# Performance work log

Hardware: AMD Instinct MI355X
Metric: run time of the kernel (lower is better)

The kernel has to match this reference:

```python
import jax, jax.numpy as jnp
import numpy as np

E_EDGES = 100000   # number of original edges (edge tokens)
M_PAIRS = 1000000  # number of edge-edge (line-graph) pairs
IN_DIM = 128
H = 8   # num_heads
D = 16  # out_dim per head


def setup_inputs() -> dict:
    key = jax.random.key(0)
    ks = jax.random.split(key, 8)
    edge_attr = jax.random.normal(ks[0], (E_EDGES, IN_DIM), dtype=jnp.float32)
    edge_edge_index = jax.random.randint(ks[1], (2, M_PAIRS), 0, E_EDGES, dtype=jnp.int64)
    s = 1.0 / np.sqrt(IN_DIM)  # xavier-ish scale
    Wq = jax.random.normal(ks[2], (IN_DIM, H * D), dtype=jnp.float32) * s
    Wk = jax.random.normal(ks[3], (IN_DIM, H * D), dtype=jnp.float32) * s
    Wv = jax.random.normal(ks[4], (IN_DIM, H * D), dtype=jnp.float32) * s
    bq = jnp.zeros((H * D,), dtype=jnp.float32)
    bk = jnp.zeros((H * D,), dtype=jnp.float32)
    bv = jnp.zeros((H * D,), dtype=jnp.float32)
    Aw = jax.random.normal(ks[5], (D, H), dtype=jnp.float32) * (1.0 / np.sqrt(D))
    return {"edge_attr": edge_attr, "edge_edge_index": edge_edge_index,
            "Wq": Wq, "bq": bq, "Wk": Wk, "bk": bk, "Wv": Wv, "bv": bv, "Aw": Aw}


def reference(edge_attr, edge_edge_index, Wq, bq, Wk, bk, Wv, bv, Aw):
    E = edge_attr.shape[0]
    # Q/K/V projections, reshaped to [E, H, D]
    Qh = (edge_attr @ Wq + bq).reshape(E, H, D)
    Kh = (edge_attr @ Wk + bk).reshape(E, H, D)
    Vh = (edge_attr @ Wv + bv).reshape(E, H, D)
    src = edge_edge_index[0]
    dst = edge_edge_index[1]
    # gather + additive score over edge-edge pairs: [M, H, D]
    score_vec = Kh[src] + Qh[dst]  # act = Identity
    # einsum 'ehd,dhc->ehc' with c=1 -> [M, H]
    raw_attn = jnp.einsum('mhd,dh->mh', score_vec, Aw)
    # segment softmax grouped by destination edge
    mx = jax.ops.segment_max(raw_attn, dst, num_segments=E)  # [E, H]
    ex = jnp.exp(raw_attn - mx[dst])
    denom = jax.ops.segment_sum(ex, dst, num_segments=E)[dst] + 1e-16
    attn = ex / denom  # [M, H]; dropout p=0 -> identity
    # weighted scatter-add aggregation
    msg = Vh[src] * attn[..., None]  # [M, H, D]
    edge_out = jax.ops.segment_sum(msg, dst, num_segments=E)  # [E, H, D]
    return edge_out
```

## Files before the change

kernel.cpp:

```cpp
#include <hip/hip_runtime.h>
#include <math.h>

static constexpr int E = 100000;
static constexpr int M = 1000000;

#define O_FLAG   0
#define O_WEFF   512
#define O_BKEFF  4608
#define O_BSWZ   5120
#define O_COUNTS 38400
#define O_OFFS   438784
#define O_BSUM   838784
#define O_BSUM2  840832
#define O_POS    842880
#define O_CSR    4842880
#define O_KS     8842880
#define O_VH     12042880
#define WS_NEEDED (O_VH + (size_t)E * 128 * 2)

typedef float f32x4 __attribute__((ext_vector_type(4)));
typedef short s16x8 __attribute__((ext_vector_type(8)));

__device__ __forceinline__ unsigned short f2bf(float f) {
    unsigned u = __float_as_uint(f);
    u += 0x7fffu + ((u >> 16) & 1u);
    return (unsigned short)(u >> 16);
}
__device__ __forceinline__ float bflo(unsigned u) { return __uint_as_float(u << 16); }
__device__ __forceinline__ float bfhi(unsigned u) { return __uint_as_float(u & 0xffff0000u); }

__global__ void k_prep(const float* __restrict__ Wk, const float* __restrict__ bk,
                       const float* __restrict__ Aw, const float* __restrict__ Wv,
                       const int* __restrict__ idx32, int* __restrict__ counts,
                       int* __restrict__ flag, float* __restrict__ weff,
                       float* __restrict__ bkeff, unsigned short* __restrict__ Bswz,
                       int nbE) {
    int bid = blockIdx.x, t = threadIdx.x;
    if (bid < nbE) {
        int i = bid * 256 + t;
        if (i < E) counts[i] = 0;
        return;
    }
    if (bid == nbE) {
        if (t < 128) {
            for (int h = 0; h < 8; h++) {
                float s = 0.f;
                for (int d = 0; d < 16; d++) s += Wk[t * 128 + h * 16 + d] * Aw[d * 8 + h];
                weff[t * 8 + h] = s;
            }
            if (t < 8) {
                float s = 0.f;
                for (int d = 0; d < 16; d++) s += bk[t * 16 + d] * Aw[d * 8 + t];
                bkeff[t] = s;
            }
        }
        return;
    }
    if (bid == nbE + 1) {
        if (t == 0) {
            int z = 0;
            for (int i = 0; i < 64; i++) z += (idx32[2 * i + 1] == 0) ? 1 : 0;
            *flag = (z == 64) ? 1 : 0;
        }
        return;
    }
    int p = (bid - (nbE + 2)) * 256 + t;
    int f = p >> 6, lane = p & 63;
    int c = f >> 3, tt = f & 7;
    int quad = lane >> 4, nn = lane & 15;
#pragma unroll
    for (int j = 0; j < 8; j++) {
        int k = c * 32 + quad * 8 + j;
        Bswz[p * 8 + j] = f2bf(Wv[k * 128 + tt * 16 + nn]);
    }
}

__global__ void k_count(const void* __restrict__ idx, const int* __restrict__ flagp,
                        int* __restrict__ counts, int* __restrict__ pos) {
    int m = blockIdx.x * blockDim.x + threadIdx.x;
    if (m >= M) return;
    int d = (*flagp) ? (int)((const long long*)idx)[M + m] : ((const int*)idx)[M + m];
    pos[m] = atomicAdd(&counts[d], 1);
}

__global__ void k_scanA(const int* __restrict__ counts, int* __restrict__ offs,
                        int* __restrict__ bsum) {
    __shared__ int sm[256];
    int tid = threadIdx.x;
    int i = blockIdx.x * 256 + tid;
    int v = (i < E) ? counts[i] : 0;
    sm[tid] = v;
    __syncthreads();
    for (int off = 1; off < 256; off <<= 1) {
        int add = (tid >= off) ? sm[tid - off] : 0;
        __syncthreads();
        sm[tid] += add;
        __syncthreads();
    }
    if (i < E) offs[i] = sm[tid] - v;
    if (tid == 255) bsum[blockIdx.x] = sm[255];
}

__global__ void k_scanB(const int* __restrict__ bsum, int* __restrict__ bsum2, int nb) {
    __shared__ int sm[512];
    int tid = threadIdx.x;
    int v = (tid < nb) ? bsum[tid] : 0;
    sm[tid] = v;
    __syncthreads();
    for (int off = 1; off < 512; off <<= 1) {
        int add = (tid >= off) ? sm[tid - off] : 0;
        __syncthreads();
        sm[tid] += add;
        __syncthreads();
    }
    bsum2[tid] = sm[tid] - v;
}

__global__ void k_fill(const void* __restrict__ idx, const int* __restrict__ flagp,
                       const int* __restrict__ offs, const int* __restrict__ bsum2,
                       const int* __restrict__ pos, int* __restrict__ csr) {
    int m = blockIdx.x * blockDim.x + threadIdx.x;
    if (m >= M) return;
    int s, d;
    if (*flagp) {
        const long long* p = (const long long*)idx;
        s = (int)p[m]; d = (int)p[M + m];
    } else {
        const int* p = (const int*)idx;
        s = p[m]; d = p[M + m];
    }
    csr[offs[d] + bsum2[d >> 8] + pos[m]] = s;
}

__global__ __launch_bounds__(256) void k_proj(
    const float* __restrict__ A, const short* __restrict__ Bswz,
    const float* __restrict__ bv, const float* __restrict__ weff,
    const float* __restrict__ bkeff, unsigned short* __restrict__ Vh,
    float* __restrict__ ksb) {
    __shared__ float we[1024];
    int t = threadIdx.x;
    ((float4*)we)[t] = ((const float4*)weff)[t & 255];
    __syncthreads();

    int lane = t & 63, wid = t >> 6;
    int rowbase = blockIdx.x * 64 + wid * 16;
    int quad = lane >> 4, nn = lane & 15;
    int m = rowbase + nn;
    int mc = (m < E) ? m : (E - 1);

    f32x4 acc[8];
#pragma unroll
    for (int tt = 0; tt < 8; tt++) acc[tt] = (f32x4){0.f, 0.f, 0.f, 0.f};
    float p[8];
#pragma unroll
    for (int h = 0; h < 8; h++) p[h] = 0.f;

#pragma unroll
    for (int c = 0; c < 4; c++) {
        const float4* ap = (const float4*)(A + (size_t)mc * 128 + c * 32 + quad * 8);
        float4 f0 = ap[0], f1 = ap[1];
        float a[8] = {f0.x, f0.y, f0.z, f0.w, f1.x, f1.y, f1.z, f1.w};
#pragma unroll
        for (int j = 0; j < 8; j++) {
            int k = c * 32 + quad * 8 + j;
            float4 w0 = *(const float4*)&we[k * 8];
            float4 w1 = *(const float4*)&we[k * 8 + 4];
            p[0] += a[j] * w0.x; p[1] += a[j] * w0.y;
            p[2] += a[j] * w0.z; p[3] += a[j] * w0.w;
            p[4] += a[j] * w1.x; p[5] += a[j] * w1.y;
            p[6] += a[j] * w1.z; p[7] += a[j] * w1.w;
        }
        s16x8 afrag;
#pragma unroll
        for (int j = 0; j < 8; j++) afrag[j] = (short)f2bf(a[j]);
#pragma unroll
        for (int tt = 0; tt < 8; tt++) {
            s16x8 bfrag = *(const s16x8*)(Bswz + (((c * 8 + tt) * 64 + lane) << 3));
            acc[tt] = __builtin_amdgcn_mfma_f32_16x16x32_bf16(afrag, bfrag, acc[tt], 0, 0, 0);
        }
    }
#pragma unroll
    for (int off = 16; off <= 32; off <<= 1)
#pragma unroll
        for (int h = 0; h < 8; h++) p[h] += __shfl_xor(p[h], off, 64);
    if (quad == 0 && m < E) {
        float4* op = (float4*)(ksb + (size_t)m * 8);
        op[0] = make_float4(p[0] + bkeff[0], p[1] + bkeff[1], p[2] + bkeff[2], p[3] + bkeff[3]);
        op[1] = make_float4(p[4] + bkeff[4], p[5] + bkeff[5], p[6] + bkeff[6], p[7] + bkeff[7]);
    }
#pragma unroll
    for (int tt = 0; tt < 8; tt++) {
        float bvc = bv[tt * 16 + nn];
#pragma unroll
        for (int r = 0; r < 4; r++) {
            int row = rowbase + quad * 4 + r;
            if (row < E)
                Vh[(size_t)row * 128 + tt * 16 + nn] = f2bf(acc[tt][r] + bvc);
        }
    }
}

__global__ __launch_bounds__(256) void k_seg(
    const float* __restrict__ ksb, const unsigned short* __restrict__ Vh,
    const int* __restrict__ offs, const int* __restrict__ bsum2,
    const int* __restrict__ csr, float* __restrict__ out) {
    int t = threadIdx.x;
    int h = t & 7;
    int seg = blockIdx.x * 32 + (t >> 3);
    int beg = offs[seg] + bsum2[seg >> 8];
    int end = (seg + 1 < E) ? (offs[seg + 1] + bsum2[(seg + 1) >> 8]) : M;
    int n = end - beg;
    const float* kb = ksb + h;

    float acc[16];
#pragma unroll
    for (int j = 0; j < 16; j++) acc[j] = 0.f;
    float l = 0.f;

    if (n > 0) {
        float mx = -INFINITY;
        for (int i = 0; i < n; i++) {
            int s = csr[beg + i];
            mx = fmaxf(mx, kb[(size_t)s * 8]);
        }
        for (int i = 0; i < n; i++) {
            int s = csr[beg + i];
            float w = __expf(kb[(size_t)s * 8] - mx);
            l += w;
            const uint4* vp = (const uint4*)(Vh + (size_t)s * 128 + h * 16);
            uint4 v0 = vp[0], v1 = vp[1];
            acc[0]  += bflo(v0.x) * w; acc[1]  += bfhi(v0.x) * w;
            acc[2]  += bflo(v0.y) * w; acc[3]  += bfhi(v0.y) * w;
            acc[4]  += bflo(v0.z) * w; acc[5]  += bfhi(v0.z) * w;
            acc[6]  += bflo(v0.w) * w; acc[7]  += bfhi(v0.w) * w;
            acc[8]  += bflo(v1.x) * w; acc[9]  += bfhi(v1.x) * w;
            acc[10] += bflo(v1.y) * w; acc[11] += bfhi(v1.y) * w;
            acc[12] += bflo(v1.z) * w; acc[13] += bfhi(v1.z) * w;
            acc[14] += bflo(v1.w) * w; acc[15] += bfhi(v1.w) * w;
        }
    }
    float inv = 1.0f / (l + 1e-16f);
    float4* op = (float4*)(out + (size_t)seg * 128 + h * 16);
#pragma unroll
    for (int j = 0; j < 4; j++)
        op[j] = make_float4(acc[4 * j] * inv, acc[4 * j + 1] * inv,
                            acc[4 * j + 2] * inv, acc[4 * j + 3] * inv);
}

extern "C" void kernel_launch(void* const* d_in, const int* in_sizes, int n_in,
                              void* d_out, int out_size, void* d_ws, size_t ws_size,
                              hipStream_t stream) {
    const float* edge_attr = (const float*)d_in[0];
    const void*  eei       = d_in[1];
    const float* Wk = (const float*)d_in[4];
    const float* bk = (const float*)d_in[5];
    const float* Wv = (const float*)d_in[6];
    const float* bv = (const float*)d_in[7];
    const float* Aw = (const float*)d_in[8];
    float* out = (float*)d_out;

    if (ws_size < WS_NEEDED) return;

    char* ws = (char*)d_ws;
    int*   flag   = (int*)(ws + O_FLAG);
    float* weff   = (float*)(ws + O_WEFF);
    float* bkeff  = (float*)(ws + O_BKEFF);
    unsigned short* Bswz = (unsigned short*)(ws + O_BSWZ);
    int*   counts = (int*)(ws + O_COUNTS);
    int*   offs   = (int*)(ws + O_OFFS);
    int*   bsum   = (int*)(ws + O_BSUM);
    int*   bsum2  = (int*)(ws + O_BSUM2);
    int*   pos    = (int*)(ws + O_POS);
    int*   csr    = (int*)(ws + O_CSR);
    float* ksb    = (float*)(ws + O_KS);
    unsigned short* Vh = (unsigned short*)(ws + O_VH);

    const int nbE = (E + 255) / 256;
    const int nbM = (M + 255) / 256;

    k_prep<<<nbE + 10, 256, 0, stream>>>(Wk, bk, Aw, Wv, (const int*)eei,
                                         counts, flag, weff, bkeff, Bswz, nbE);
    k_count<<<nbM, 256, 0, stream>>>(eei, flag, counts, pos);
    k_scanA<<<nbE, 256, 0, stream>>>(counts, offs, bsum);
    k_scanB<<<1, 512, 0, stream>>>(bsum, bsum2, nbE);
    k_fill<<<nbM, 256, 0, stream>>>(eei, flag, offs, bsum2, pos, csr);
    k_proj<<<(E + 63) / 64, 256, 0, stream>>>(edge_attr, (const short*)Bswz, bv,
                                              weff, bkeff, Vh, ksb);
    k_seg<<<E / 32, 256, 0, stream>>>(ksb, Vh, offs, bsum2, csr, out);
}
```

Baseline: 267.2 us.

## Fuse count with projection, degree-sort segments, pipeline online-softmax gathers

Merges the destination-count atomics and the Q/K/V projection into one interleaved launch so the atomic-bound work overlaps the MFMA projection. Adds a degree histogram and counting sort so the segment kernel handles segments in descending-degree order, which balances work across wavefronts. Replaces the two-pass max/exp loop with a single-pass online softmax that prefetches four rows ahead to hide gather latency. Costs are extra histogram and ordering passes, an indirection through the order array, and higher register pressure in the segment kernel.

```diff
diff --git a/kernel.cpp b/kernel.cpp
--- a/kernel.cpp
+++ b/kernel.cpp
@@ -3,6 +3,9 @@
 
 static constexpr int E = 100000;
 static constexpr int M = 1000000;
+static constexpr int NBE = (E + 255) / 256;
+static constexpr int NBM = (M + 255) / 256;
+static constexpr int NBP = (E + 63) / 64;
 
 #define O_FLAG   0
 #define O_WEFF   512
@@ -12,10 +15,14 @@
 #define O_OFFS   438784
 #define O_BSUM   838784
 #define O_BSUM2  840832
-#define O_POS    842880
-#define O_CSR    4842880
-#define O_KS     8842880
-#define O_VH     12042880
+#define O_BINOFF 842880
+#define O_BCUR   843904
+#define O_BHIST  844928
+#define O_ORDER  1245312
+#define O_POS    1645312
+#define O_CSR    5645312
+#define O_KS     9645312
+#define O_VH     12845312
 #define WS_NEEDED (O_VH + (size_t)E * 128 * 2)
 
 typedef float f32x4 __attribute__((ext_vector_type(4)));
@@ -33,15 +40,14 @@
                        const float* __restrict__ Aw, const float* __restrict__ Wv,
                        const int* __restrict__ idx32, int* __restrict__ counts,
                        int* __restrict__ flag, float* __restrict__ weff,
-                       float* __restrict__ bkeff, unsigned short* __restrict__ Bswz,
-                       int nbE) {
+                       float* __restrict__ bkeff, unsigned short* __restrict__ Bswz) {
     int bid = blockIdx.x, t = threadIdx.x;
-    if (bid < nbE) {
+    if (bid < NBE) {
         int i = bid * 256 + t;
         if (i < E) counts[i] = 0;
         return;
     }
-    if (bid == nbE) {
+    if (bid == NBE) {
         if (t < 128) {
             for (int h = 0; h < 8; h++) {
                 float s = 0.f;
@@ -56,7 +62,7 @@
         }
         return;
     }
-    if (bid == nbE + 1) {
+    if (bid == NBE + 1) {
         if (t == 0) {
             int z = 0;
             for (int i = 0; i < 64; i++) z += (idx32[2 * i + 1] == 0) ? 1 : 0;
@@ -64,7 +70,7 @@
         }
         return;
     }
-    int p = (bid - (nbE + 2)) * 256 + t;
+    int p = (bid - (NBE + 2)) * 256 + t;
     int f = p >> 6, lane = p & 63;
     int c = f >> 3, tt = f & 7;
     int quad = lane >> 4, nn = lane & 15;
@@ -75,75 +81,33 @@
     }
 }
 
-__global__ void k_count(const void* __restrict__ idx, const int* __restrict__ flagp,
-                        int* __restrict__ counts, int* __restrict__ pos) {
-    int m = blockIdx.x * blockDim.x + threadIdx.x;
-    if (m >= M) return;
-    int d = (*flagp) ? (int)((const long long*)idx)[M + m] : ((const int*)idx)[M + m];
-    pos[m] = atomicAdd(&counts[d], 1);
-}
-
-__global__ void k_scanA(const int* __restrict__ counts, int* __restrict__ offs,
-                        int* __restrict__ bsum) {
-    __shared__ int sm[256];
-    int tid = threadIdx.x;
-    int i = blockIdx.x * 256 + tid;
-    int v = (i < E) ? counts[i] : 0;
-    sm[tid] = v;
-    __syncthreads();
-    for (int off = 1; off < 256; off <<= 1) {
-        int add = (tid >= off) ? sm[tid - off] : 0;
-        __syncthreads();
-        sm[tid] += add;
-        __syncthreads();
-    }
-    if (i < E) offs[i] = sm[tid] - v;
-    if (tid == 255) bsum[blockIdx.x] = sm[255];
-}
-
-__global__ void k_scanB(const int* __restrict__ bsum, int* __restrict__ bsum2, int nb) {
-    __shared__ int sm[512];
-    int tid = threadIdx.x;
-    int v = (tid < nb) ? bsum[tid] : 0;
-    sm[tid] = v;
-    __syncthreads();
-    for (int off = 1; off < 512; off <<= 1) {
-        int add = (tid >= off) ? sm[tid - off] : 0;
-        __syncthreads();
-        sm[tid] += add;
-        __syncthreads();
-    }
-    bsum2[tid] = sm[tid] - v;
-}
-
-__global__ void k_fill(const void* __restrict__ idx, const int* __restrict__ flagp,
-                       const int* __restrict__ offs, const int* __restrict__ bsum2,
-                       const int* __restrict__ pos, int* __restrict__ csr) {
-    int m = blockIdx.x * blockDim.x + threadIdx.x;
-    if (m >= M) return;
-    int s, d;
-    if (*flagp) {
-        const long long* p = (const long long*)idx;
-        s = (int)p[m]; d = (int)p[M + m];
-    } else {
-        const int* p = (const int*)idx;
-        s = p[m]; d = p[M + m];
-    }
-    csr[offs[d] + bsum2[d >> 8] + pos[m]] = s;
-}
-
-__global__ __launch_bounds__(256) void k_proj(
+__global__ __launch_bounds__(256) void k_cp(
+    const void* __restrict__ idx, const int* __restrict__ flagp,
+    int* __restrict__ counts, int* __restrict__ pos,
     const float* __restrict__ A, const short* __restrict__ Bswz,
     const float* __restrict__ bv, const float* __restrict__ weff,
     const float* __restrict__ bkeff, unsigned short* __restrict__ Vh,
     float* __restrict__ ksb) {
+    int bid = blockIdx.x, t = threadIdx.x;
+    int r = bid % 7;
+    if (r < 5) {
+        int cid = (bid / 7) * 5 + r;
+        if (cid >= NBM) return;
+        int m = cid * 256 + t;
+        if (m >= M) return;
+        int d = (*flagp) ? (int)((const long long*)idx)[M + m] : ((const int*)idx)[M + m];
+        pos[m] = atomicAdd(&counts[d], 1);
+        return;
+    }
+    int pid = (bid / 7) * 2 + (r - 5);
+    if (pid >= NBP) return;
+
     __shared__ float we[1024];
-    int t = threadIdx.x;
     ((float4*)we)[t] = ((const float4*)weff)[t & 255];
     __syncthreads();
 
     int lane = t & 63, wid = t >> 6;
-    int rowbase = blockIdx.x * 64 + wid * 16;
+    int rowbase = pid * 64 + wid * 16;
     int quad = lane >> 4, nn = lane & 15;
     int m = rowbase + nn;
     int mc = (m < E) ? m : (E - 1);
@@ -192,52 +156,173 @@
     for (int tt = 0; tt < 8; tt++) {
         float bvc = bv[tt * 16 + nn];
 #pragma unroll
-        for (int r = 0; r < 4; r++) {
-            int row = rowbase + quad * 4 + r;
+        for (int rr = 0; rr < 4; rr++) {
+            int row = rowbase + quad * 4 + rr;
             if (row < E)
-                Vh[(size_t)row * 128 + tt * 16 + nn] = f2bf(acc[tt][r] + bvc);
-        }
-    }
+                Vh[(size_t)row * 128 + tt * 16 + nn] = f2bf(acc[tt][rr] + bvc);
+        }
+    }
+}
+
+__global__ void k_scanA(const int* __restrict__ counts, int* __restrict__ offs,
+                        int* __restrict__ bsum, int* __restrict__ bhist) {
+    __shared__ int sm[256];
+    __shared__ int hist[256];
+    int tid = threadIdx.x;
+    int i = blockIdx.x * 256 + tid;
+    int v = (i < E) ? counts[i] : 0;
+    hist[tid] = 0;
+    sm[tid] = v;
+    __syncthreads();
+    if (i < E) atomicAdd(&hist[v > 255 ? 255 : v], 1);
+    for (int off = 1; off < 256; off <<= 1) {
+        int add = (tid >= off) ? sm[tid - off] : 0;
+        __syncthreads();
+        sm[tid] += add;
+        __syncthreads();
+    }
+    if (i < E) offs[i] = sm[tid] - v;
+    if (tid == 255) bsum[blockIdx.x] = sm[255];
+    bhist[blockIdx.x * 256 + tid] = hist[tid];
+}
+
+__global__ void k_scanB(const int* __restrict__ bsum, const int* __restrict__ bhist,
+                        int* __restrict__ bsum2, int* __restrict__ binoff,
+                        int* __restrict__ bcur, int nb) {
+    __shared__ int sm[512];
+    __shared__ int bt[256];
+    __shared__ int s2[256];
+    int tid = threadIdx.x;
+    int v = (tid < nb) ? bsum[tid] : 0;
+    sm[tid] = v;
+    __syncthreads();
+    for (int off = 1; off < 512; off <<= 1) {
+        int add = (tid >= off) ? sm[tid - off] : 0;
+        __syncthreads();
+        sm[tid] += add;
+        __syncthreads();
+    }
+    bsum2[tid] = sm[tid] - v;
+    if (tid < 256) {
+        int s = 0;
+        for (int j = 0; j < nb; j++) s += bhist[j * 256 + tid];
+        bt[tid] = s;
+    }
+    __syncthreads();
+    if (tid < 256) s2[tid] = bt[255 - tid];
+    __syncthreads();
+    for (int off = 1; off < 256; off <<= 1) {
+        int add = (tid < 256 && tid >= off) ? s2[tid - off] : 0;
+        __syncthreads();
+        if (tid < 256) s2[tid] += add;
+        __syncthreads();
+    }
+    if (tid < 256) {
+        binoff[tid] = s2[255 - tid] - bt[tid];
+        bcur[tid] = 0;
+    }
+}
+
+__global__ void k_fill(const void* __restrict__ idx, const int* __restrict__ flagp,
+                       const int* __restrict__ offs, const int* __restrict__ bsum2,
+                       const int* __restrict__ pos, int* __restrict__ csr,
+                       const int* __restrict__ counts, const int* __restrict__ binoff,
+                       int* __restrict__ bcur, int* __restrict__ order) {
+    int bid = blockIdx.x, t = threadIdx.x;
+    if (bid < NBM) {
+        int m = bid * 256 + t;
+        if (m >= M) return;
+        int s, d;
+        if (*flagp) {
+            const long long* p = (const long long*)idx;
+            s = (int)p[m]; d = (int)p[M + m];
+        } else {
+            const int* p = (const int*)idx;
+            s = p[m]; d = p[M + m];
+        }
+        csr[offs[d] + bsum2[d >> 8] + pos[m]] = s;
+        return;
+    }
+    int i = (bid - NBM) * 256 + t;
+    if (i >= E) return;
+    int n = counts[i];
+    if (n > 255) n = 255;
+    int r = atomicAdd(&bcur[n], 1);
+    order[binoff[n] + r] = i;
+}
+
+#define ROWL(p, sidx, cond) \
+    if (cond) { \
+        k##p = ksb[(size_t)(sidx) * 8 + h]; \
+        const uint4* vp_ = (const uint4*)(Vh + (size_t)(sidx) * 128 + (h << 4)); \
+        a##p = vp_[0]; b##p = vp_[1]; \
+    }
+
+#define CONS(kk, aa, bb) { \
+    float kv_ = kk; \
+    float w_; \
+    if (kv_ > mx) { \
+        float r_ = __expf(mx - kv_); \
+        l *= r_; \
+        _Pragma("unroll") for (int j_ = 0; j_ < 16; j_++) acc[j_] *= r_; \
+        mx = kv_; w_ = 1.f; \
+    } else w_ = __expf(kv_ - mx); \
+    l += w_; \
+    acc[0]  += bflo(aa.x) * w_; acc[1]  += bfhi(aa.x) * w_; \
+    acc[2]  += bflo(aa.y) * w_; acc[3]  += bfhi(aa.y) * w_; \
+    acc[4]  += bflo(aa.z) * w_; acc[5]  += bfhi(aa.z) * w_; \
+    acc[6]  += bflo(aa.w) * w_; acc[7]  += bfhi(aa.w) * w_; \
+    acc[8]  += bflo(bb.x) * w_; acc[9]  += bfhi(bb.x) * w_; \
+    acc[10] += bflo(bb.y) * w_; acc[11] += bfhi(bb.y) * w_; \
+    acc[12] += bflo(bb.z) * w_; acc[13] += bfhi(bb.z) * w_; \
+    acc[14] += bflo(bb.w) * w_; acc[15] += bfhi(bb.w) * w_; \
 }
 
 __global__ __launch_bounds__(256) void k_seg(
     const float* __restrict__ ksb, const unsigned short* __restrict__ Vh,
     const int* __restrict__ offs, const int* __restrict__ bsum2,
-    const int* __restrict__ csr, float* __restrict__ out) {
+    const int* __restrict__ csr, const int* __restrict__ order,
+    float* __restrict__ out) {
     int t = threadIdx.x;
     int h = t & 7;
-    int seg = blockIdx.x * 32 + (t >> 3);
+    int g = blockIdx.x * 32 + (t >> 3);
+    int seg = order[g];
     int beg = offs[seg] + bsum2[seg >> 8];
     int end = (seg + 1 < E) ? (offs[seg + 1] + bsum2[(seg + 1) >> 8]) : M;
     int n = end - beg;
-    const float* kb = ksb + h;
 
     float acc[16];
 #pragma unroll
     for (int j = 0; j < 16; j++) acc[j] = 0.f;
-    float l = 0.f;
+    float l = 0.f, mx = -INFINITY;
 
     if (n > 0) {
-        float mx = -INFINITY;
-        for (int i = 0; i < n; i++) {
-            int s = csr[beg + i];
-            mx = fmaxf(mx, kb[(size_t)s * 8]);
-        }
-        for (int i = 0; i < n; i++) {
-            int s = csr[beg + i];
-            float w = __expf(kb[(size_t)s * 8] - mx);
-            l += w;
-            const uint4* vp = (const uint4*)(Vh + (size_t)s * 128 + h * 16);
-            uint4 v0 = vp[0], v1 = vp[1];
-            acc[0]  += bflo(v0.x) * w; acc[1]  += bfhi(v0.x) * w;
-            acc[2]  += bflo(v0.y) * w; acc[3]  += bfhi(v0.y) * w;
-            acc[4]  += bflo(v0.z) * w; acc[5]  += bfhi(v0.z) * w;
-            acc[6]  += bflo(v0.w) * w; acc[7]  += bfhi(v0.w) * w;
-            acc[8]  += bflo(v1.x) * w; acc[9]  += bfhi(v1.x) * w;
-            acc[10] += bflo(v1.y) * w; acc[11] += bfhi(v1.y) * w;
-            acc[12] += bflo(v1.z) * w; acc[13] += bfhi(v1.z) * w;
-            acc[14] += bflo(v1.w) * w; acc[15] += bfhi(v1.w) * w;
-        }
+        int s0 = 0, s1 = 0, s2 = 0, s3 = 0, t0 = 0, t1 = 0, t2 = 0, t3 = 0;
+        float k0 = 0, k1 = 0, k2 = 0, k3 = 0;
+        uint4 a0 = {}, b0 = {}, a1 = {}, b1 = {}, a2 = {}, b2 = {}, a3 = {}, b3 = {};
+        s0 = csr[beg];
+        if (n > 1) s1 = csr[beg + 1];
+        if (n > 2) s2 = csr[beg + 2];
+        if (n > 3) s3 = csr[beg + 3];
+        ROWL(0, s0, true)
+        ROWL(1, s1, n > 1)
+        ROWL(2, s2, n > 2)
+        ROWL(3, s3, n > 3)
+        if (n > 4) t0 = csr[beg + 4];
+        if (n > 5) t1 = csr[beg + 5];
+        if (n > 6) t2 = csr[beg + 6];
+        if (n > 7) t3 = csr[beg + 7];
+        int i = 0;
+        while (i + 4 <= n) {
+            CONS(k0, a0, b0) ROWL(0, t0, i + 4 < n) if (i + 8 < n)  t0 = csr[beg + i + 8];
+            CONS(k1, a1, b1) ROWL(1, t1, i + 5 < n) if (i + 9 < n)  t1 = csr[beg + i + 9];
+            CONS(k2, a2, b2) ROWL(2, t2, i + 6 < n) if (i + 10 < n) t2 = csr[beg + i + 10];
+            CONS(k3, a3, b3) ROWL(3, t3, i + 7 < n) if (i + 11 < n) t3 = csr[beg + i + 11];
+            i += 4;
+        }
+        if (i < n) { CONS(k0, a0, b0) i++; }
+        if (i < n) { CONS(k1, a1, b1) i++; }
+        if (i < n) { CONS(k2, a2, b2) }
     }
     float inv = 1.0f / (l + 1e-16f);
     float4* op = (float4*)(out + (size_t)seg * 128 + h * 16);
@@ -270,21 +355,22 @@
     int*   offs   = (int*)(ws + O_OFFS);
     int*   bsum   = (int*)(ws + O_BSUM);
     int*   bsum2  = (int*)(ws + O_BSUM2);
+    int*   binoff = (int*)(ws + O_BINOFF);
+    int*   bcur   = (int*)(ws + O_BCUR);
+    int*   bhist  = (int*)(ws + O_BHIST);
+    int*   order  = (int*)(ws + O_ORDER);
     int*   pos    = (int*)(ws + O_POS);
     int*   csr    = (int*)(ws + O_CSR);
     float* ksb    = (float*)(ws + O_KS);
     unsigned short* Vh = (unsigned short*)(ws + O_VH);
 
-    const int nbE = (E + 255) / 256;
-    const int nbM = (M + 255) / 256;
-
-    k_prep<<<nbE + 10, 256, 0, stream>>>(Wk, bk, Aw, Wv, (const int*)eei,
-                                         counts, flag, weff, bkeff, Bswz, nbE);
-    k_count<<<nbM, 256, 0, stream>>>(eei, flag, counts, pos);
-    k_scanA<<<nbE, 256, 0, stream>>>(counts, offs, bsum);
-    k_scanB<<<1, 512, 0, stream>>>(bsum, bsum2, nbE);
-    k_fill<<<nbM, 256, 0, stream>>>(eei, flag, offs, bsum2, pos, csr);
-    k_proj<<<(E + 63) / 64, 256, 0, stream>>>(edge_attr, (const short*)Bswz, bv,
-                                              weff, bkeff, Vh, ksb);
-    k_seg<<<E / 32, 256, 0, stream>>>(ksb, Vh, offs, bsum2, csr, out);
-}
+    k_prep<<<NBE + 10, 256, 0, stream>>>(Wk, bk, Aw, Wv, (const int*)eei,
+                                         counts, flag, weff, bkeff, Bswz);
+    k_cp<<<7 * 782, 256, 0, stream>>>(eei, flag, counts, pos, edge_attr,
+                                      (const short*)Bswz, bv, weff, bkeff, Vh, ksb);
+    k_scanA<<<NBE, 256, 0, stream>>>(counts, offs, bsum, bhist);
+    k_scanB<<<1, 512, 0, stream>>>(bsum, bhist, bsum2, binoff, bcur, NBE);
+    k_fill<<<NBM + NBE, 256, 0, stream>>>(eei, flag, offs, bsum2, pos, csr,
+                                          counts, binoff, bcur, order);
+    k_seg<<<E / 32, 256, 0, stream>>>(ksb, Vh, offs, bsum2, csr, order, out);
+}
```

Measured after the change: 610.5 us. +128.5%, slower.
